# Kernel optimization log

Hardware: AMD Instinct MI355X
Metric: run time of the kernel (lower is better)

The kernel has to match this reference:

```python
import jax, jax.numpy as jnp
import numpy as np

N, D = 4096, 2048

def setup_inputs() -> dict:
    key = jax.random.key(0)
    k1, k2 = jax.random.split(key)
    Ws = jax.random.normal(k1, (N, D), dtype=jnp.float32)
    # nn.Bilinear(D, D, 1): weight [1, D, D], bias [1]
    W = jax.random.normal(k2, (1, D, D), dtype=jnp.float32) * (1.0 / np.sqrt(D))
    b = jnp.zeros((1,), dtype=jnp.float32)
    return {"Ws": Ws, "W": W, "b": b}

def reference(Ws, W, b):
    # A[i, j] = Ws[i] @ W[0] @ Ws[j] + b[0]  (bilinear score for every pair)
    t = Ws @ W[0]                 # [N, D]
    A = t @ Ws.T + b[0]           # [N, N]
    return jax.nn.softmax(A, axis=1)
```

## Files before the change

### kernel.cpp

```cpp
#include <hip/hip_runtime.h>

typedef __bf16 bf16x8 __attribute__((ext_vector_type(8)));
typedef float f32x4 __attribute__((ext_vector_type(4)));
typedef unsigned short u16;
typedef u16 u16x8 __attribute__((ext_vector_type(8)));

#define AS1 __attribute__((address_space(1)))
#define AS3 __attribute__((address_space(3)))

__device__ __forceinline__ void split2(float x, u16& h, u16& l) {
  __bf16 hb = (__bf16)x;
  float hf = (float)hb;
  __bf16 lb = (__bf16)(x - hf);
  h = __builtin_bit_cast(u16, hb);
  l = __builtin_bit_cast(u16, lb);
}

__global__ __launch_bounds__(256) void k_pack_ws(const float* __restrict__ X,
                                                 u16* __restrict__ P) {
  const int total8 = (4096 * 2048) / 8;
  for (int idx = blockIdx.x * 256 + threadIdx.x; idx < total8; idx += gridDim.x * 256) {
    int row = idx >> 8;
    int k8  = idx & 255;
    const float* src = X + ((size_t)row << 11) + (k8 << 3);
    const float4 v0 = *(const float4*)src;
    const float4 v1 = *(const float4*)(src + 4);
    float xv[8] = {v0.x, v0.y, v0.z, v0.w, v1.x, v1.y, v1.z, v1.w};
    u16x8 hv, lv;
#pragma unroll
    for (int j = 0; j < 8; ++j) { u16 h, l; split2(xv[j], h, l); hv[j] = h; lv[j] = l; }
    size_t base = ((size_t)row << 12) + (size_t)((k8 >> 2) << 6) + ((k8 & 3) << 3);
    *(u16x8*)(P + base) = hv;
    *(u16x8*)(P + base + 32) = lv;
  }
}

__global__ __launch_bounds__(256) void k_transpose_pack_w(const float* __restrict__ W,
                                                          u16* __restrict__ P) {
  __shared__ float tile[32][33];
  const int tx = threadIdx.x, ty = threadIdx.y;
  const int kbase = blockIdx.y << 5, cbase = blockIdx.x << 5;
#pragma unroll
  for (int i = 0; i < 4; ++i)
    tile[ty * 4 + i][tx] = W[((size_t)(kbase + ty * 4 + i) << 11) + cbase + tx];
  __syncthreads();
#pragma unroll
  for (int i = 0; i < 4; ++i) {
    int c = cbase + ty * 4 + i;
    float v = tile[tx][ty * 4 + i];
    u16 h, l; split2(v, h, l);
    size_t base = ((size_t)c << 12) + (size_t)(kbase << 1) + tx;
    P[base] = h;
    P[base + 32] = l;
  }
}

template <bool SPLIT_OUT>
__global__ __launch_bounds__(256, 2) void k_gemm_nt(const u16* __restrict__ Ap,
                                                    const u16* __restrict__ Bp,
                                                    float* __restrict__ Cout,
                                                    u16* __restrict__ Cpack,
                                                    const int Ncols) {
  __shared__ __align__(16) u16 lds_a[128 * 64];
  __shared__ __align__(16) u16 lds_b[128 * 64];
  const int tid = threadIdx.x;
  const int lane = tid & 63, w = tid >> 6;
  const int wr = w >> 1, wc = w & 1;
  const int row0 = blockIdx.y << 7, col0 = blockIdx.x << 7;
  const int lrow = lane & 15, kg = lane >> 4;

  f32x4 acc[4][4] = {};

  const u16* abase = Ap + ((size_t)row0 << 12);
  const u16* bbase = Bp + ((size_t)col0 << 12);

  int offAh[4], offAl[4], offBh[4], offBl[4];
#pragma unroll
  for (int m = 0; m < 4; ++m) {
    int r = wr * 64 + m * 16 + lrow;
    int sw = r & 7;
    offAh[m] = r * 64 + ((kg ^ sw) << 3);
    offAl[m] = r * 64 + (((4 + kg) ^ sw) << 3);
    int rb = wc * 64 + m * 16 + lrow;
    int swb = rb & 7;
    offBh[m] = rb * 64 + ((kg ^ swb) << 3);
    offBl[m] = rb * 64 + (((4 + kg) ^ swb) << 3);
  }

  for (int kb = 0; kb < 64; ++kb) {
    const int kofs = kb << 6;
#pragma unroll
    for (int i = 0; i < 4; ++i) {
      int s = i * 256 + tid;
      int r = s >> 3, c = s & 7;
      int cs = c ^ (r & 7);
      __builtin_amdgcn_global_load_lds(
          (const AS1 unsigned int*)(abase + ((size_t)r << 12) + kofs + (cs << 3)),
          (AS3 unsigned int*)(lds_a + ((i * 256 + w * 64) << 3)), 16, 0, 0);
    }
#pragma unroll
    for (int i = 0; i < 4; ++i) {
      int s = i * 256 + tid;
      int r = s >> 3, c = s & 7;
      int cs = c ^ (r & 7);
      __builtin_amdgcn_global_load_lds(
          (const AS1 unsigned int*)(bbase + ((size_t)r << 12) + kofs + (cs << 3)),
          (AS3 unsigned int*)(lds_b + ((i * 256 + w * 64) << 3)), 16, 0, 0);
    }
    __syncthreads();

    bf16x8 ah[4], al[4];
#pragma unroll
    for (int m = 0; m < 4; ++m) {
      ah[m] = *(const bf16x8*)&lds_a[offAh[m]];
      al[m] = *(const bf16x8*)&lds_a[offAl[m]];
    }
#pragma unroll
    for (int n = 0; n < 4; ++n) {
      bf16x8 bh = *(const bf16x8*)&lds_b[offBh[n]];
      bf16x8 bl = *(const bf16x8*)&lds_b[offBl[n]];
#pragma unroll
      for (int m = 0; m < 4; ++m) {
        acc[m][n] = __builtin_amdgcn_mfma_f32_16x16x32_bf16(ah[m], bh, acc[m][n], 0, 0, 0);
        acc[m][n] = __builtin_amdgcn_mfma_f32_16x16x32_bf16(ah[m], bl, acc[m][n], 0, 0, 0);
        acc[m][n] = __builtin_amdgcn_mfma_f32_16x16x32_bf16(al[m], bh, acc[m][n], 0, 0, 0);
      }
    }
    __syncthreads();
  }

#pragma unroll
  for (int m = 0; m < 4; ++m) {
#pragma unroll
    for (int n = 0; n < 4; ++n) {
#pragma unroll
      for (int j = 0; j < 4; ++j) {
        int gr = row0 + wr * 64 + m * 16 + kg * 4 + j;
        int gc = col0 + wc * 64 + n * 16 + lrow;
        float x = acc[m][n][j];
        if (SPLIT_OUT) {
          u16 h, l; split2(x, h, l);
          size_t base = ((size_t)gr << 12) + (size_t)((gc >> 5) << 6) + (gc & 31);
          Cpack[base] = h;
          Cpack[base + 32] = l;
        } else {
          Cout[(size_t)gr * Ncols + gc] = x;
        }
      }
    }
  }
}

__global__ __launch_bounds__(512, 2) void k_gemm256(const u16* __restrict__ Ap,
                                                    const u16* __restrict__ Bp,
                                                    float* __restrict__ Cout) {
  __shared__ __align__(16) u16 sm[65536];
  const int tid = threadIdx.x;
  const int lane = tid & 63, w = tid >> 6;
  const int wr = w >> 2, wc = w & 3;
  const int row0 = blockIdx.y << 8, col0 = blockIdx.x << 8;
  const int lrow = lane & 15, kg = lane >> 4;
  const int sw = lrow & 7;

  const u16* Abase = Ap + ((size_t)row0 << 12);
  const u16* Bbase = Bp + ((size_t)col0 << 12);

  const size_t gsrc0 = ((size_t)(tid >> 3) << 12) + ((size_t)((tid & 7) ^ ((tid >> 3) & 7)) << 3);
  const int dst0 = (w * 64) << 3;

  auto stA = [&](int T, int j) {
    __builtin_amdgcn_global_load_lds(
        (const AS1 unsigned int*)(Abase + gsrc0 + ((size_t)(j * 64) << 12) + ((T & 63) << 6)),
        (AS3 unsigned int*)(sm + ((T & 1) << 14) + j * 4096 + dst0), 16, 0, 0);
  };
  auto stB = [&](int T, int j) {
    __builtin_amdgcn_global_load_lds(
        (const AS1 unsigned int*)(Bbase + gsrc0 + ((size_t)(j * 64) << 12) + ((T & 63) << 6)),
        (AS3 unsigned int*)(sm + 32768 + ((T & 1) << 14) + j * 4096 + dst0), 16, 0, 0);
  };

  const int baseAh = wr * 8192 + lrow * 64 + ((kg ^ sw) << 3);
  const int baseAl = wr * 8192 + lrow * 64 + (((4 | kg) ^ sw) << 3);
  const int baseBh = (wc * 64 + lrow) * 64 + ((kg ^ sw) << 3);
  const int baseBl = (wc * 64 + lrow) * 64 + (((4 | kg) ^ sw) << 3);

  f32x4 acc[8][4] = {};
  bf16x8 bh[4], bl[4];

  stA(0, 0); stA(0, 1); stA(0, 2); stA(0, 3);
  stB(0, 0); stB(0, 1); stB(0, 2); stB(0, 3);
  stB(1, 0); stB(1, 1); stB(1, 2); stB(1, 3);
  stA(1, 0); stA(1, 2);
  asm volatile("s_waitcnt vmcnt(6)" ::: "memory");
  __builtin_amdgcn_sched_barrier(0);
  __builtin_amdgcn_s_barrier();

  for (int i = 0; i < 32; ++i) {
    const int t0 = 2 * i;
#pragma unroll
    for (int p = 0; p < 8; ++p) {
      const int q = p & 3;
      const int t = t0 + (p >> 2);
      const u16* la = sm + ((t & 1) << 14);
      const u16* lb = sm + 32768 + ((t & 1) << 14);
      if (q == 0) {
#pragma unroll
        for (int n = 0; n < 4; ++n) {
          bh[n] = *(const bf16x8*)&lb[baseBh + n * 1024];
          bl[n] = *(const bf16x8*)&lb[baseBl + n * 1024];
        }
      }
      bf16x8 ah0 = *(const bf16x8*)&la[baseAh + (2 * q) * 1024];
      bf16x8 al0 = *(const bf16x8*)&la[baseAl + (2 * q) * 1024];
      bf16x8 ah1 = *(const bf16x8*)&la[baseAh + (2 * q + 1) * 1024];
      bf16x8 al1 = *(const bf16x8*)&la[baseAl + (2 * q + 1) * 1024];
      switch (p) {
        case 0: stA(t0 + 1, 1); stA(t0 + 1, 3); break;
        case 1: stB(t0 + 2, 0); stB(t0 + 2, 1); break;
        case 2: stB(t0 + 2, 2); stB(t0 + 2, 3); break;
        case 3: stA(t0 + 2, 0); stA(t0 + 2, 2); break;
        case 4: stA(t0 + 2, 1); stA(t0 + 2, 3); break;
        case 5: stB(t0 + 3, 0); stB(t0 + 3, 1); break;
        case 6: stB(t0 + 3, 2); stB(t0 + 3, 3); break;
        case 7: stA(t0 + 3, 0); stA(t0 + 3, 2); break;
      }
      __builtin_amdgcn_s_barrier();
      __builtin_amdgcn_s_setprio(1);
      const int m0 = 2 * q, m1 = 2 * q + 1;
#pragma unroll
      for (int n = 0; n < 4; ++n) {
        acc[m0][n] = __builtin_amdgcn_mfma_f32_16x16x32_bf16(ah0, bh[n], acc[m0][n], 0, 0, 0);
        acc[m1][n] = __builtin_amdgcn_mfma_f32_16x16x32_bf16(ah1, bh[n], acc[m1][n], 0, 0, 0);
      }
#pragma unroll
      for (int n = 0; n < 4; ++n) {
        acc[m0][n] = __builtin_amdgcn_mfma_f32_16x16x32_bf16(ah0, bl[n], acc[m0][n], 0, 0, 0);
        acc[m1][n] = __builtin_amdgcn_mfma_f32_16x16x32_bf16(ah1, bl[n], acc[m1][n], 0, 0, 0);
      }
#pragma unroll
      for (int n = 0; n < 4; ++n) {
        acc[m0][n] = __builtin_amdgcn_mfma_f32_16x16x32_bf16(al0, bh[n], acc[m0][n], 0, 0, 0);
        acc[m1][n] = __builtin_amdgcn_mfma_f32_16x16x32_bf16(al1, bh[n], acc[m1][n], 0, 0, 0);
      }
      __builtin_amdgcn_s_setprio(0);
      asm volatile("s_waitcnt lgkmcnt(0)" ::: "memory");
      __builtin_amdgcn_sched_barrier(0);
      if (q == 3) {
        asm volatile("s_waitcnt vmcnt(6)" ::: "memory");
        __builtin_amdgcn_sched_barrier(0);
      }
      __builtin_amdgcn_s_barrier();
    }
  }
  asm volatile("s_waitcnt vmcnt(0)" ::: "memory");

#pragma unroll
  for (int m = 0; m < 8; ++m) {
#pragma unroll
    for (int n = 0; n < 4; ++n) {
#pragma unroll
      for (int j = 0; j < 4; ++j) {
        int gr = row0 + wr * 128 + m * 16 + kg * 4 + j;
        int gc = col0 + wc * 64 + n * 16 + lrow;
        Cout[((size_t)gr << 12) + gc] = acc[m][n][j];
      }
    }
  }
}

__global__ __launch_bounds__(256) void k_softmax_rows(float* __restrict__ A) {
  const int row = blockIdx.x;
  float* p = A + ((size_t)row << 12);
  const int tid = threadIdx.x;
  const int lane = tid & 63, w = tid >> 6;
  float4 v[4];
  float mx = -3.0e38f;
#pragma unroll
  for (int i = 0; i < 4; ++i) {
    v[i] = ((const float4*)p)[tid + (i << 8)];
    mx = fmaxf(mx, fmaxf(fmaxf(v[i].x, v[i].y), fmaxf(v[i].z, v[i].w)));
  }
#pragma unroll
  for (int off = 32; off; off >>= 1) mx = fmaxf(mx, __shfl_xor(mx, off, 64));
  __shared__ float redm[4], reds[4];
  if (lane == 0) redm[w] = mx;
  __syncthreads();
  mx = fmaxf(fmaxf(redm[0], redm[1]), fmaxf(redm[2], redm[3]));
  float s = 0.f;
#pragma unroll
  for (int i = 0; i < 4; ++i) {
    v[i].x = __expf(v[i].x - mx);
    v[i].y = __expf(v[i].y - mx);
    v[i].z = __expf(v[i].z - mx);
    v[i].w = __expf(v[i].w - mx);
    s += (v[i].x + v[i].y) + (v[i].z + v[i].w);
  }
#pragma unroll
  for (int off = 32; off; off >>= 1) s += __shfl_xor(s, off, 64);
  if (lane == 0) reds[w] = s;
  __syncthreads();
  s = (reds[0] + reds[1]) + (reds[2] + reds[3]);
  const float inv = 1.0f / s;
#pragma unroll
  for (int i = 0; i < 4; ++i) {
    v[i].x *= inv; v[i].y *= inv; v[i].z *= inv; v[i].w *= inv;
    ((float4*)p)[tid + (i << 8)] = v[i];
  }
}

extern "C" void kernel_launch(void* const* d_in, const int* in_sizes, int n_in,
                              void* d_out, int out_size, void* d_ws, size_t ws_size,
                              hipStream_t stream) {
  (void)in_sizes; (void)n_in; (void)out_size; (void)ws_size;
  const float* Ws = (const float*)d_in[0];
  const float* W  = (const float*)d_in[1];
  float* out = (float*)d_out;

  u16* ws_pack = (u16*)d_ws;
  u16* wt_pack = ws_pack + (size_t)4096 * 4096;
  u16* t_pack  = wt_pack + (size_t)2048 * 4096;

  k_pack_ws<<<4096, 256, 0, stream>>>(Ws, ws_pack);
  k_transpose_pack_w<<<dim3(64, 64), dim3(32, 8), 0, stream>>>(W, wt_pack);
  k_gemm_nt<true><<<dim3(16, 32), 256, 0, stream>>>(ws_pack, wt_pack, nullptr, t_pack, 2048);
  k_gemm256<<<dim3(16, 16), 512, 0, stream>>>(t_pack, ws_pack, out);
  k_softmax_rows<<<4096, 256, 0, stream>>>(out);
}
```

Before: 263.6 us.

## Load B fragments directly to registers and swizzle block order for XCD locality

The main 256x256 GEMM stops staging the B operand through LDS. Each wave now loads its own B fragments straight from global memory into double-buffered registers (even/odd k-steps), while A keeps its LDS double buffer. This halves LDS usage and LDS read traffic and simplifies the async-copy schedule, at the cost of more VGPRs and uncoalesced per-wave global reads whose latency must be hidden by the vmcnt waits. Both GEMMs also switch to 1D grids with a block-index swizzle that groups tiles per XCD for better L2 reuse, and the unused template path in the first GEMM is removed.

```diff
diff --git a/kernel.cpp b/kernel.cpp
--- a/kernel.cpp
+++ b/kernel.cpp
@@ -7,6 +7,7 @@
 
 #define AS1 __attribute__((address_space(1)))
 #define AS3 __attribute__((address_space(3)))
+#define MF(d, a, b) d = __builtin_amdgcn_mfma_f32_16x16x32_bf16(a, b, d, 0, 0, 0)
 
 __device__ __forceinline__ void split2(float x, u16& h, u16& l) {
   __bf16 hb = (__bf16)x;
@@ -55,18 +56,18 @@
   }
 }
 
-template <bool SPLIT_OUT>
 __global__ __launch_bounds__(256, 2) void k_gemm_nt(const u16* __restrict__ Ap,
                                                     const u16* __restrict__ Bp,
-                                                    float* __restrict__ Cout,
-                                                    u16* __restrict__ Cpack,
-                                                    const int Ncols) {
+                                                    u16* __restrict__ Cpack) {
   __shared__ __align__(16) u16 lds_a[128 * 64];
   __shared__ __align__(16) u16 lds_b[128 * 64];
+  const int bid = blockIdx.x;
+  const int swzb = (bid & 7) * 64 + (bid >> 3);
+  const int bx = swzb & 15, by = swzb >> 4;
   const int tid = threadIdx.x;
   const int lane = tid & 63, w = tid >> 6;
   const int wr = w >> 1, wc = w & 1;
-  const int row0 = blockIdx.y << 7, col0 = blockIdx.x << 7;
+  const int row0 = by << 7, col0 = bx << 7;
   const int lrow = lane & 15, kg = lane >> 4;
 
   f32x4 acc[4][4] = {};
@@ -121,9 +122,9 @@
       bf16x8 bl = *(const bf16x8*)&lds_b[offBl[n]];
 #pragma unroll
       for (int m = 0; m < 4; ++m) {
-        acc[m][n] = __builtin_amdgcn_mfma_f32_16x16x32_bf16(ah[m], bh, acc[m][n], 0, 0, 0);
-        acc[m][n] = __builtin_amdgcn_mfma_f32_16x16x32_bf16(ah[m], bl, acc[m][n], 0, 0, 0);
-        acc[m][n] = __builtin_amdgcn_mfma_f32_16x16x32_bf16(al[m], bh, acc[m][n], 0, 0, 0);
+        MF(acc[m][n], ah[m], bh);
+        MF(acc[m][n], ah[m], bl);
+        MF(acc[m][n], al[m], bh);
       }
     }
     __syncthreads();
@@ -137,15 +138,10 @@
       for (int j = 0; j < 4; ++j) {
         int gr = row0 + wr * 64 + m * 16 + kg * 4 + j;
         int gc = col0 + wc * 64 + n * 16 + lrow;
-        float x = acc[m][n][j];
-        if (SPLIT_OUT) {
-          u16 h, l; split2(x, h, l);
-          size_t base = ((size_t)gr << 12) + (size_t)((gc >> 5) << 6) + (gc & 31);
-          Cpack[base] = h;
-          Cpack[base + 32] = l;
-        } else {
-          Cout[(size_t)gr * Ncols + gc] = x;
-        }
+        u16 h, l; split2(acc[m][n][j], h, l);
+        size_t base = ((size_t)gr << 12) + (size_t)((gc >> 5) << 6) + (gc & 31);
+        Cpack[base] = h;
+        Cpack[base + 32] = l;
       }
     }
   }
@@ -154,11 +150,14 @@
 __global__ __launch_bounds__(512, 2) void k_gemm256(const u16* __restrict__ Ap,
                                                     const u16* __restrict__ Bp,
                                                     float* __restrict__ Cout) {
-  __shared__ __align__(16) u16 sm[65536];
+  __shared__ __align__(16) u16 smA[32768];
+  const int bid = blockIdx.x;
+  const int swzb = (bid & 7) * 32 + (bid >> 3);
+  const int bx = swzb & 15, by = swzb >> 4;
   const int tid = threadIdx.x;
   const int lane = tid & 63, w = tid >> 6;
   const int wr = w >> 2, wc = w & 3;
-  const int row0 = blockIdx.y << 8, col0 = blockIdx.x << 8;
+  const int row0 = by << 8, col0 = bx << 8;
   const int lrow = lane & 15, kg = lane >> 4;
   const int sw = lrow & 7;
 
@@ -171,82 +170,84 @@
   auto stA = [&](int T, int j) {
     __builtin_amdgcn_global_load_lds(
         (const AS1 unsigned int*)(Abase + gsrc0 + ((size_t)(j * 64) << 12) + ((T & 63) << 6)),
-        (AS3 unsigned int*)(sm + ((T & 1) << 14) + j * 4096 + dst0), 16, 0, 0);
+        (AS3 unsigned int*)(smA + ((T & 1) << 14) + j * 4096 + dst0), 16, 0, 0);
   };
-  auto stB = [&](int T, int j) {
-    __builtin_amdgcn_global_load_lds(
-        (const AS1 unsigned int*)(Bbase + gsrc0 + ((size_t)(j * 64) << 12) + ((T & 63) << 6)),
-        (AS3 unsigned int*)(sm + 32768 + ((T & 1) << 14) + j * 4096 + dst0), 16, 0, 0);
+  auto ldB = [&](int T, bf16x8* BH, bf16x8* BL) {
+    const u16* src = Bbase + ((T & 63) << 6) + (kg << 3);
+#pragma unroll
+    for (int n = 0; n < 4; ++n) {
+      size_t c = (size_t)(wc * 64 + n * 16 + lrow) << 12;
+      BH[n] = *(const bf16x8*)(src + c);
+      BL[n] = *(const bf16x8*)(src + c + 32);
+    }
   };
 
-  const int baseAh = wr * 8192 + lrow * 64 + ((kg ^ sw) << 3);
-  const int baseAl = wr * 8192 + lrow * 64 + (((4 | kg) ^ sw) << 3);
-  const int baseBh = (wc * 64 + lrow) * 64 + ((kg ^ sw) << 3);
-  const int baseBl = (wc * 64 + lrow) * 64 + (((4 | kg) ^ sw) << 3);
+  const int baseAh = (wr * 128 + lrow) * 64 + ((kg ^ sw) << 3);
+  const int baseAl = (wr * 128 + lrow) * 64 + (((4 | kg) ^ sw) << 3);
 
   f32x4 acc[8][4] = {};
-  bf16x8 bh[4], bl[4];
+  bf16x8 bhE[4], blE[4], bhO[4], blO[4];
 
   stA(0, 0); stA(0, 1); stA(0, 2); stA(0, 3);
-  stB(0, 0); stB(0, 1); stB(0, 2); stB(0, 3);
-  stB(1, 0); stB(1, 1); stB(1, 2); stB(1, 3);
-  stA(1, 0); stA(1, 2);
-  asm volatile("s_waitcnt vmcnt(6)" ::: "memory");
+  ldB(0, bhE, blE);
+  ldB(1, bhO, blO);
+  __builtin_amdgcn_sched_barrier(0);
+  asm volatile("s_waitcnt vmcnt(8)" ::: "memory");
   __builtin_amdgcn_sched_barrier(0);
   __builtin_amdgcn_s_barrier();
 
   for (int i = 0; i < 32; ++i) {
     const int t0 = 2 * i;
-#pragma unroll
-    for (int p = 0; p < 8; ++p) {
-      const int q = p & 3;
-      const int t = t0 + (p >> 2);
-      const u16* la = sm + ((t & 1) << 14);
-      const u16* lb = sm + 32768 + ((t & 1) << 14);
-      if (q == 0) {
-#pragma unroll
-        for (int n = 0; n < 4; ++n) {
-          bh[n] = *(const bf16x8*)&lb[baseBh + n * 1024];
-          bl[n] = *(const bf16x8*)&lb[baseBl + n * 1024];
-        }
-      }
-      bf16x8 ah0 = *(const bf16x8*)&la[baseAh + (2 * q) * 1024];
-      bf16x8 al0 = *(const bf16x8*)&la[baseAl + (2 * q) * 1024];
-      bf16x8 ah1 = *(const bf16x8*)&la[baseAh + (2 * q + 1) * 1024];
-      bf16x8 al1 = *(const bf16x8*)&la[baseAl + (2 * q + 1) * 1024];
-      switch (p) {
-        case 0: stA(t0 + 1, 1); stA(t0 + 1, 3); break;
-        case 1: stB(t0 + 2, 0); stB(t0 + 2, 1); break;
-        case 2: stB(t0 + 2, 2); stB(t0 + 2, 3); break;
-        case 3: stA(t0 + 2, 0); stA(t0 + 2, 2); break;
-        case 4: stA(t0 + 2, 1); stA(t0 + 2, 3); break;
-        case 5: stB(t0 + 3, 0); stB(t0 + 3, 1); break;
-        case 6: stB(t0 + 3, 2); stB(t0 + 3, 3); break;
-        case 7: stA(t0 + 3, 0); stA(t0 + 3, 2); break;
-      }
+    const u16* laE = smA;
+    const u16* laO = smA + 16384;
+#pragma unroll
+    for (int q = 0; q < 4; ++q) {
+      bf16x8 a0h = *(const bf16x8*)&laE[baseAh + (2 * q) * 1024];
+      bf16x8 a0l = *(const bf16x8*)&laE[baseAl + (2 * q) * 1024];
+      bf16x8 a1h = *(const bf16x8*)&laE[baseAh + (2 * q + 1) * 1024];
+      bf16x8 a1l = *(const bf16x8*)&laE[baseAl + (2 * q + 1) * 1024];
+      if (q == 0) { stA(t0 + 1, 0); stA(t0 + 1, 1); }
+      if (q == 1) { stA(t0 + 1, 2); stA(t0 + 1, 3); }
       __builtin_amdgcn_s_barrier();
       __builtin_amdgcn_s_setprio(1);
       const int m0 = 2 * q, m1 = 2 * q + 1;
 #pragma unroll
-      for (int n = 0; n < 4; ++n) {
-        acc[m0][n] = __builtin_amdgcn_mfma_f32_16x16x32_bf16(ah0, bh[n], acc[m0][n], 0, 0, 0);
-        acc[m1][n] = __builtin_amdgcn_mfma_f32_16x16x32_bf16(ah1, bh[n], acc[m1][n], 0, 0, 0);
-      }
-#pragma unroll
-      for (int n = 0; n < 4; ++n) {
-        acc[m0][n] = __builtin_amdgcn_mfma_f32_16x16x32_bf16(ah0, bl[n], acc[m0][n], 0, 0, 0);
-        acc[m1][n] = __builtin_amdgcn_mfma_f32_16x16x32_bf16(ah1, bl[n], acc[m1][n], 0, 0, 0);
-      }
-#pragma unroll
-      for (int n = 0; n < 4; ++n) {
-        acc[m0][n] = __builtin_amdgcn_mfma_f32_16x16x32_bf16(al0, bh[n], acc[m0][n], 0, 0, 0);
-        acc[m1][n] = __builtin_amdgcn_mfma_f32_16x16x32_bf16(al1, bh[n], acc[m1][n], 0, 0, 0);
-      }
+      for (int n = 0; n < 4; ++n) { MF(acc[m0][n], a0h, bhE[n]); MF(acc[m1][n], a1h, bhE[n]); }
+#pragma unroll
+      for (int n = 0; n < 4; ++n) { MF(acc[m0][n], a0h, blE[n]); MF(acc[m1][n], a1h, blE[n]); }
+#pragma unroll
+      for (int n = 0; n < 4; ++n) { MF(acc[m0][n], a0l, bhE[n]); MF(acc[m1][n], a1l, bhE[n]); }
       __builtin_amdgcn_s_setprio(0);
-      asm volatile("s_waitcnt lgkmcnt(0)" ::: "memory");
-      __builtin_amdgcn_sched_barrier(0);
       if (q == 3) {
-        asm volatile("s_waitcnt vmcnt(6)" ::: "memory");
+        ldB(t0 + 2, bhE, blE);
+        __builtin_amdgcn_sched_barrier(0);
+        asm volatile("s_waitcnt vmcnt(8)" ::: "memory");
+        __builtin_amdgcn_sched_barrier(0);
+      }
+      __builtin_amdgcn_s_barrier();
+    }
+#pragma unroll
+    for (int q = 0; q < 4; ++q) {
+      bf16x8 a0h = *(const bf16x8*)&laO[baseAh + (2 * q) * 1024];
+      bf16x8 a0l = *(const bf16x8*)&laO[baseAl + (2 * q) * 1024];
+      bf16x8 a1h = *(const bf16x8*)&laO[baseAh + (2 * q + 1) * 1024];
+      bf16x8 a1l = *(const bf16x8*)&laO[baseAl + (2 * q + 1) * 1024];
+      if (q == 0) { stA(t0 + 2, 0); stA(t0 + 2, 1); }
+      if (q == 1) { stA(t0 + 2, 2); stA(t0 + 2, 3); }
+      __builtin_amdgcn_s_barrier();
+      __builtin_amdgcn_s_setprio(1);
+      const int m0 = 2 * q, m1 = 2 * q + 1;
+#pragma unroll
+      for (int n = 0; n < 4; ++n) { MF(acc[m0][n], a0h, bhO[n]); MF(acc[m1][n], a1h, bhO[n]); }
+#pragma unroll
+      for (int n = 0; n < 4; ++n) { MF(acc[m0][n], a0h, blO[n]); MF(acc[m1][n], a1h, blO[n]); }
+#pragma unroll
+      for (int n = 0; n < 4; ++n) { MF(acc[m0][n], a0l, bhO[n]); MF(acc[m1][n], a1l, bhO[n]); }
+      __builtin_amdgcn_s_setprio(0);
+      if (q == 3) {
+        ldB(t0 + 3, bhO, blO);
+        __builtin_amdgcn_sched_barrier(0);
+        asm volatile("s_waitcnt vmcnt(8)" ::: "memory");
         __builtin_amdgcn_sched_barrier(0);
       }
       __builtin_amdgcn_s_barrier();
@@ -322,7 +323,7 @@
 
   k_pack_ws<<<4096, 256, 0, stream>>>(Ws, ws_pack);
   k_transpose_pack_w<<<dim3(64, 64), dim3(32, 8), 0, stream>>>(W, wt_pack);
-  k_gemm_nt<true><<<dim3(16, 32), 256, 0, stream>>>(ws_pack, wt_pack, nullptr, t_pack, 2048);
-  k_gemm256<<<dim3(16, 16), 512, 0, stream>>>(t_pack, ws_pack, out);
+  k_gemm_nt<<<512, 256, 0, stream>>>(ws_pack, wt_pack, t_pack);
+  k_gemm256<<<256, 512, 0, stream>>>(t_pack, ws_pack, out);
   k_softmax_rows<<<4096, 256, 0, stream>>>(out);
 }
```

New measurement: 322.5 us. +22.4%, slower.
